# Kernel tuning notes

Measured on AMD Instinct MI355X. Metric: run time of the kernel, lower is better.

The kernel has to match this reference:

```python
import jax, jax.numpy as jnp
import numpy as np
import math

C = 512
D = C // 4  # 128
SCALE = math.sqrt(D)

def setup_inputs() -> dict:
    key = jax.random.key(0)
    k1, k2, k3, k4 = jax.random.split(key, 4)
    x = jax.random.normal(k1, (8, C, 2048), dtype=jnp.float32)
    # q_conv and k_conv share the same weight (tied in the torch module)
    wqk = jax.random.normal(k2, (D, C), dtype=jnp.float32) * (1.0 / math.sqrt(C))
    wv = jax.random.normal(k3, (D, C), dtype=jnp.float32) * (1.0 / math.sqrt(C))
    bv = jax.random.normal(k4, (D,), dtype=jnp.float32) * 0.01
    return {"x": x, "wqk": wqk, "wv": wv, "bv": bv}

def reference(x, wqk, wv, bv):
    # x: [B, C, N]; 1x1 conv == matmul over channel dim
    xq = jnp.einsum('dc,bcn->bnd', wqk, x)          # [B, N, D]
    xk = jnp.einsum('dc,bcn->bdn', wqk, x)          # [B, D, N]
    xv = jnp.einsum('dc,bcn->bdn', wv, x) + bv[None, :, None]  # [B, D, N]
    energy = jnp.einsum('bnd,bdm->bnm', xq, xk) / SCALE  # [B, N, N]
    attention = jax.nn.softmax(energy, axis=-1)
    x_r = jnp.einsum('bdn,bnm->bdm', xv, attention)  # [B, D, N]
    return x_r
```

## Files before the change

kernel.cpp:

```cpp
#include <hip/hip_runtime.h>

typedef short short4v __attribute__((ext_vector_type(4)));
typedef short short8 __attribute__((ext_vector_type(8)));
typedef float floatx4 __attribute__((ext_vector_type(4)));
typedef unsigned int uint;
typedef unsigned short ushort;

#define CH 512
#define NN 2048
#define DD 128
#define RSCALE 0.08838834764831845f

__device__ __forceinline__ float bf2f(ushort u) {
    union { uint i; float f; } v; v.i = ((uint)u) << 16; return v.f;
}
__device__ __forceinline__ ushort f2bf(float f) {
    union { float f; uint u; } v; v.f = f;
    uint u = v.u;
    return (ushort)((u + 0x7fffu + ((u >> 16) & 1u)) >> 16);
}

__global__ __launch_bounds__(256) void k0_prep(
    const float* __restrict__ wqk, const float* __restrict__ wv,
    ushort* __restrict__ Wbf, float* __restrict__ lsum,
    float* __restrict__ out)
{
    int gid = blockIdx.x * 256 + threadIdx.x;
    if (gid < 32768) {
        int base = gid * 4;
        const float* src = (base < 65536) ? (wqk + base) : (wv + base - 65536);
        float4 v = *(const float4*)src;
        short4v o;
        o[0] = (short)f2bf(v.x); o[1] = (short)f2bf(v.y);
        o[2] = (short)f2bf(v.z); o[3] = (short)f2bf(v.w);
        *(short4v*)&Wbf[base] = o;
    }
    if (gid < 16384) lsum[gid] = 0.0f;
    float4 z; z.x = 0.f; z.y = 0.f; z.z = 0.f; z.w = 0.f;
#pragma unroll
    for (int i = 0; i < 4; i++)
        *(float4*)&out[(size_t)(gid + i * 131072) * 4] = z;
}

__global__ __launch_bounds__(256) void k1_proj(
    const float* __restrict__ x,
    const ushort* __restrict__ Wbf,
    const float* __restrict__ bv,
    ushort* __restrict__ Q,
    ushort* __restrict__ VT)
{
    const int nt = blockIdx.x;
    const int h  = blockIdx.y;
    const int b  = blockIdx.z;
    const int n0 = nt * 32;
    const int t = threadIdx.x;
    const int lane = t & 63, w = t >> 6, l15 = lane & 15, quad = lane >> 4;

    __shared__ __attribute__((aligned(16))) ushort As[32 * 72];
    __shared__ __attribute__((aligned(16))) ushort Bs[128 * 72];
    __shared__ __attribute__((aligned(16))) ushort Vt[128 * 40];

    floatx4 acc[2][2];
#pragma unroll
    for (int i = 0; i < 2; i++)
#pragma unroll
        for (int j = 0; j < 2; j++) acc[i][j] = (floatx4)(0.0f);

    const float* xb = x + b * (CH * NN) + n0;
    const ushort* Wh = Wbf + h * 128 * CH;

    const int an = t & 31, ag = t >> 5;

    for (int c0 = 0; c0 < CH; c0 += 64) {
        {
            short8 v;
#pragma unroll
            for (int i = 0; i < 8; i++)
                v[i] = (short)f2bf(xb[(c0 + ag * 8 + i) * NN + an]);
            *(short8*)&As[an * 72 + ag * 8] = v;
        }
#pragma unroll
        for (int rep = 0; rep < 4; rep++) {
            int idx = rep * 256 + t;
            int row = idx >> 3, g = idx & 7;
            *(short8*)&Bs[row * 72 + g * 8] = *(const short8*)&Wh[row * CH + c0 + g * 8];
        }
        __syncthreads();
#pragma unroll
        for (int kd = 0; kd < 2; kd++) {
            short8 a0 = *(short8*)&As[(l15) * 72 + kd * 32 + quad * 8];
            short8 a1 = *(short8*)&As[(16 + l15) * 72 + kd * 32 + quad * 8];
#pragma unroll
            for (int dt2 = 0; dt2 < 2; dt2++) {
                short8 bf = *(short8*)&Bs[(w * 32 + dt2 * 16 + l15) * 72 + kd * 32 + quad * 8];
                acc[0][dt2] = __builtin_amdgcn_mfma_f32_16x16x32_bf16(a0, bf, acc[0][dt2], 0, 0, 0);
                acc[1][dt2] = __builtin_amdgcn_mfma_f32_16x16x32_bf16(a1, bf, acc[1][dt2], 0, 0, 0);
            }
        }
        __syncthreads();
    }

#pragma unroll
    for (int ns = 0; ns < 2; ns++)
#pragma unroll
        for (int dt2 = 0; dt2 < 2; dt2++) {
            int ds_ = w * 32 + dt2 * 16 + l15;
#pragma unroll
            for (int r = 0; r < 4; r++) {
                int nl = ns * 16 + quad * 4 + r;
                float val = acc[ns][dt2][r];
                if (h == 0) {
                    Q[b * (NN * DD) + (n0 + nl) * DD + ds_] = f2bf(val);
                } else {
                    Vt[ds_ * 40 + nl] = f2bf(val + bv[ds_]);
                }
            }
        }
    if (h == 1) {
        __syncthreads();
#pragma unroll
        for (int rep = 0; rep < 2; rep++) {
            int idx = rep * 256 + t;
            int dv = idx >> 2, seg = idx & 3;
            *(short8*)&VT[((size_t)b * DD + dv) * NN + n0 + seg * 8] =
                *(short8*)&Vt[dv * 40 + seg * 8];
        }
    }
}

__global__ __launch_bounds__(256, 4) void k_p(
    const ushort* __restrict__ Q,
    ushort* __restrict__ P,
    float* __restrict__ lsum)
{
    int pid = blockIdx.x;
    const int b = blockIdx.y;
    int it = 0;
    while (pid >= (16 - it)) { pid -= (16 - it); it++; }
    const int jt = it + pid;
    const int i0 = it * 128, j0 = jt * 128;
    const int t = threadIdx.x;
    const int lane = t & 63, w = t >> 6, l15 = lane & 15, quad = lane >> 4;
    const int wi = (w >> 1) * 64, wj = (w & 1) * 64;

    __shared__ __attribute__((aligned(16))) char smem[36864];
    ushort* Qi = (ushort*)smem;
    ushort* Qj = (ushort*)(smem + 18432);
    ushort* Pt = (ushort*)smem;

    const ushort* Qb = Q + b * (NN * DD);

    floatx4 acc[4][4];
#pragma unroll
    for (int i = 0; i < 4; i++)
#pragma unroll
        for (int j = 0; j < 4; j++) acc[i][j] = (floatx4)(0.0f);

    for (int kh = 0; kh < 2; kh++) {
        if (kh) __syncthreads();
#pragma unroll
        for (int rep = 0; rep < 4; rep++) {
            int idx = rep * 256 + t;
            int row = idx >> 3, g = idx & 7;
            *(short8*)&Qi[row * 72 + g * 8] = *(const short8*)&Qb[(i0 + row) * DD + kh * 64 + g * 8];
            *(short8*)&Qj[row * 72 + g * 8] = *(const short8*)&Qb[(j0 + row) * DD + kh * 64 + g * 8];
        }
        __syncthreads();

#pragma unroll
        for (int kd = 0; kd < 2; kd++) {
            short8 afr[4], bfr[4];
#pragma unroll
            for (int nt = 0; nt < 4; nt++)
                afr[nt] = *(short8*)&Qi[(wi + nt * 16 + l15) * 72 + kd * 32 + quad * 8];
#pragma unroll
            for (int mt = 0; mt < 4; mt++)
                bfr[mt] = *(short8*)&Qj[(wj + mt * 16 + l15) * 72 + kd * 32 + quad * 8];
#pragma unroll
            for (int nt = 0; nt < 4; nt++)
#pragma unroll
                for (int mt = 0; mt < 4; mt++)
                    acc[nt][mt] = __builtin_amdgcn_mfma_f32_16x16x32_bf16(afr[nt], bfr[mt], acc[nt][mt], 0, 0, 0);
        }
    }

    __syncthreads();

    float cs[4] = {0.f, 0.f, 0.f, 0.f};
#pragma unroll
    for (int nt = 0; nt < 4; nt++) {
        float rs[4] = {0.f, 0.f, 0.f, 0.f};
#pragma unroll
        for (int mt = 0; mt < 4; mt++)
#pragma unroll
            for (int r = 0; r < 4; r++) {
                float p = __expf(acc[nt][mt][r] * RSCALE);
                rs[r] += p;
                cs[mt] += p;
                Pt[(wi + nt * 16 + quad * 4 + r) * 138 + wj + mt * 16 + l15] = f2bf(p);
            }
#pragma unroll
        for (int r = 0; r < 4; r++) {
            float s = rs[r];
            s += __shfl_xor(s, 1);
            s += __shfl_xor(s, 2);
            s += __shfl_xor(s, 4);
            s += __shfl_xor(s, 8);
            if (l15 == 0)
                atomicAdd(&lsum[b * NN + i0 + wi + nt * 16 + quad * 4 + r], s);
        }
    }
    if (it != jt) {
#pragma unroll
        for (int mt = 0; mt < 4; mt++) {
            float s = cs[mt];
            s += __shfl_xor(s, 16);
            s += __shfl_xor(s, 32);
            if (lane < 16)
                atomicAdd(&lsum[b * NN + j0 + wj + mt * 16 + l15], s);
        }
    }
    __syncthreads();

    ushort* Pb = P + (size_t)b * NN * NN;
#pragma unroll
    for (int rep = 0; rep < 8; rep++) {
        int idx = rep * 256 + t;
        int row = idx >> 4, g = idx & 15;
        *(short8*)&Pb[(size_t)(i0 + row) * NN + j0 + g * 8] =
            *(short8*)&Pt[row * 138 + g * 8];
    }

    if (it != jt) {
        __syncthreads();
#pragma unroll
        for (int nt = 0; nt < 4; nt++)
#pragma unroll
            for (int mt = 0; mt < 4; mt++)
#pragma unroll
                for (int r = 0; r < 4; r++) {
                    float p = __expf(acc[nt][mt][r] * RSCALE);
                    Pt[(wj + mt * 16 + l15) * 138 + wi + nt * 16 + quad * 4 + r] = f2bf(p);
                }
        __syncthreads();
#pragma unroll
        for (int rep = 0; rep < 8; rep++) {
            int idx = rep * 256 + t;
            int row = idx >> 4, g = idx & 15;
            *(short8*)&Pb[(size_t)(j0 + row) * NN + i0 + g * 8] =
                *(short8*)&Pt[row * 138 + g * 8];
        }
    }
}

__global__ __launch_bounds__(256) void k_vscale(
    const ushort* __restrict__ VT, const float* __restrict__ lsum,
    ushort* __restrict__ Vsc)
{
    int gid = blockIdx.x * 256 + threadIdx.x;
    size_t idx = (size_t)gid * 8;
    int b = (int)(idx >> 18);
    int n = (int)(idx & (NN - 1));
    short8 v = *(const short8*)&VT[idx];
    float4 l0 = *(const float4*)&lsum[b * NN + n];
    float4 l1 = *(const float4*)&lsum[b * NN + n + 4];
    short8 o;
    o[0] = (short)f2bf(bf2f((ushort)v[0]) / l0.x);
    o[1] = (short)f2bf(bf2f((ushort)v[1]) / l0.y);
    o[2] = (short)f2bf(bf2f((ushort)v[2]) / l0.z);
    o[3] = (short)f2bf(bf2f((ushort)v[3]) / l0.w);
    o[4] = (short)f2bf(bf2f((ushort)v[4]) / l1.x);
    o[5] = (short)f2bf(bf2f((ushort)v[5]) / l1.y);
    o[6] = (short)f2bf(bf2f((ushort)v[6]) / l1.z);
    o[7] = (short)f2bf(bf2f((ushort)v[7]) / l1.w);
    *(short8*)&Vsc[idx] = o;
}

__global__ __launch_bounds__(256, 4) void k_pv(
    const ushort* __restrict__ Vsc,
    const ushort* __restrict__ P,
    float* __restrict__ out)
{
    const int mt = blockIdx.x;
    const int b  = blockIdx.y;
    const int m0 = mt * 32;
    const int t = threadIdx.x;
    const int lane = t & 63, w = t >> 6, l15 = lane & 15, quad = lane >> 4;

    __shared__ __attribute__((aligned(16))) ushort Vs[128 * 72];
    __shared__ __attribute__((aligned(16))) ushort Pp[32 * 72];

    const ushort* Vb = Vsc + (size_t)b * DD * NN;
    const ushort* Pb = P + (size_t)b * NN * NN;

    floatx4 acc[2][2];
#pragma unroll
    for (int i = 0; i < 2; i++)
#pragma unroll
        for (int j = 0; j < 2; j++) acc[i][j] = (floatx4)(0.0f);

    const int vsd = t >> 3, vsg = t & 7;
    const int psr = t >> 3, psg = t & 7;

    short8 vr[4], pr;

#define LOADR(NC)                                                              \
    do {                                                                       \
        _Pragma("unroll")                                                      \
        for (int rep = 0; rep < 4; rep++)                                      \
            vr[rep] = *(const short8*)&Vb[(size_t)(rep * 32 + vsd) * NN + (NC) + vsg * 8]; \
        pr = *(const short8*)&Pb[(size_t)(m0 + psr) * NN + (NC) + psg * 8];    \
    } while (0)

    LOADR(0);

    for (int n0c = 0; n0c < NN; n0c += 64) {
        __syncthreads();
#pragma unroll
        for (int rep = 0; rep < 4; rep++)
            *(short8*)&Vs[(rep * 32 + vsd) * 72 + vsg * 8] = vr[rep];
        *(short8*)&Pp[psr * 72 + psg * 8] = pr;
        __syncthreads();

        if (n0c + 64 < NN) LOADR(n0c + 64);

#pragma unroll
        for (int kn = 0; kn < 2; kn++) {
            short8 va0 = *(short8*)&Vs[(w * 32 + l15) * 72 + kn * 32 + quad * 8];
            short8 va1 = *(short8*)&Vs[(w * 32 + 16 + l15) * 72 + kn * 32 + quad * 8];
#pragma unroll
            for (int mf = 0; mf < 2; mf++) {
                short8 pb = *(short8*)&Pp[(mf * 16 + l15) * 72 + kn * 32 + quad * 8];
                acc[0][mf] = __builtin_amdgcn_mfma_f32_16x16x32_bf16(va0, pb, acc[0][mf], 0, 0, 0);
                acc[1][mf] = __builtin_amdgcn_mfma_f32_16x16x32_bf16(va1, pb, acc[1][mf], 0, 0, 0);
            }
        }
    }
#undef LOADR

    float* ob = out + (size_t)b * DD * NN;
#pragma unroll
    for (int dsub = 0; dsub < 2; dsub++)
#pragma unroll
        for (int mf = 0; mf < 2; mf++)
#pragma unroll
            for (int r = 0; r < 4; r++) {
                int d = w * 32 + dsub * 16 + quad * 4 + r;
                ob[(size_t)d * NN + m0 + mf * 16 + l15] = acc[dsub][mf][r];
            }
}

__global__ __launch_bounds__(256, 4) void kl_sum(
    const ushort* __restrict__ Q,
    float* __restrict__ lsum)
{
    int pid = blockIdx.x;
    const int b = blockIdx.y;
    int it = 0;
    while (pid >= (16 - it)) { pid -= (16 - it); it++; }
    const int jt = it + pid;
    const int i0 = it * 128, j0 = jt * 128;
    const int t = threadIdx.x;
    const int lane = t & 63, w = t >> 6, l15 = lane & 15, quad = lane >> 4;
    const int wi = (w >> 1) * 64, wj = (w & 1) * 64;

    __shared__ __attribute__((aligned(16))) ushort Qi[128 * 72];
    __shared__ __attribute__((aligned(16))) ushort Qj[128 * 72];

    const ushort* Qb = Q + b * (NN * DD);

    floatx4 acc[4][4];
#pragma unroll
    for (int i = 0; i < 4; i++)
#pragma unroll
        for (int j = 0; j < 4; j++) acc[i][j] = (floatx4)(0.0f);

    for (int kh = 0; kh < 2; kh++) {
        if (kh) __syncthreads();
#pragma unroll
        for (int rep = 0; rep < 4; rep++) {
            int idx = rep * 256 + t;
            int row = idx >> 3, g = idx & 7;
            *(short8*)&Qi[row * 72 + g * 8] = *(const short8*)&Qb[(i0 + row) * DD + kh * 64 + g * 8];
            *(short8*)&Qj[row * 72 + g * 8] = *(const short8*)&Qb[(j0 + row) * DD + kh * 64 + g * 8];
        }
        __syncthreads();

#pragma unroll
        for (int kd = 0; kd < 2; kd++) {
            short8 afr[4], bfr[4];
#pragma unroll
            for (int nt = 0; nt < 4; nt++)
                afr[nt] = *(short8*)&Qi[(wi + nt * 16 + l15) * 72 + kd * 32 + quad * 8];
#pragma unroll
            for (int mt = 0; mt < 4; mt++)
                bfr[mt] = *(short8*)&Qj[(wj + mt * 16 + l15) * 72 + kd * 32 + quad * 8];
#pragma unroll
            for (int nt = 0; nt < 4; nt++)
#pragma unroll
                for (int mt = 0; mt < 4; mt++)
                    acc[nt][mt] = __builtin_amdgcn_mfma_f32_16x16x32_bf16(afr[nt], bfr[mt], acc[nt][mt], 0, 0, 0);
        }
    }

    float cs[4] = {0.f, 0.f, 0.f, 0.f};
#pragma unroll
    for (int nt = 0; nt < 4; nt++) {
        float rs[4] = {0.f, 0.f, 0.f, 0.f};
#pragma unroll
        for (int mt = 0; mt < 4; mt++)
#pragma unroll
            for (int r = 0; r < 4; r++) {
                float p = __expf(acc[nt][mt][r] * RSCALE);
                rs[r] += p;
                cs[mt] += p;
            }
#pragma unroll
        for (int r = 0; r < 4; r++) {
            float s = rs[r];
            s += __shfl_xor(s, 1);
            s += __shfl_xor(s, 2);
            s += __shfl_xor(s, 4);
            s += __shfl_xor(s, 8);
            if (l15 == 0)
                atomicAdd(&lsum[b * NN + i0 + wi + nt * 16 + quad * 4 + r], s);
        }
    }
    if (it != jt) {
#pragma unroll
        for (int mt = 0; mt < 4; mt++) {
            float s = cs[mt];
            s += __shfl_xor(s, 16);
            s += __shfl_xor(s, 32);
            if (lane < 16)
                atomicAdd(&lsum[b * NN + j0 + wj + mt * 16 + l15], s);
        }
    }
}

__global__ __launch_bounds__(256, 4) void k_fused_sep(
    const ushort* __restrict__ Q,
    const ushort* __restrict__ VT,
    const float* __restrict__ lsum,
    float* __restrict__ out)
{
    const int mt = blockIdx.x;
    const int h  = blockIdx.y;
    const int b  = blockIdx.z;
    const int m0 = mt * 32;
    const int t = threadIdx.x;
    const int lane = t & 63, w = t >> 6, l15 = lane & 15, quad = lane >> 4;

    __shared__ __attribute__((aligned(16))) ushort Qn[64 * 136];
    __shared__ __attribute__((aligned(16))) ushort Vs[128 * 72];
    __shared__ __attribute__((aligned(16))) ushort Ps[32 * 68];

    const ushort* Qb = Q + b * (NN * DD);
    const ushort* VTb = VT + (size_t)b * DD * NN;
    const float* lb = lsum + b * NN;

#pragma unroll
    for (int rep = 0; rep < 2; rep++) {
        int idx = rep * 256 + t;
        int row = idx >> 4, g = idx & 15;
        *(short8*)&Qn[row * 136 + g * 8] = *(const short8*)&Qb[(m0 + row) * DD + g * 8];
    }
    __syncthreads();

    short8 qm[2][4];
#pragma unroll
    for (int ms = 0; ms < 2; ms++)
#pragma unroll
        for (int kd = 0; kd < 4; kd++)
            qm[ms][kd] = *(short8*)&Qn[(ms * 16 + l15) * 136 + kd * 32 + quad * 8];

    floatx4 acc[2][2];
#pragma unroll
    for (int i = 0; i < 2; i++)
#pragma unroll
        for (int j = 0; j < 2; j++) acc[i][j] = (floatx4)(0.0f);

    const int qsr = t >> 4, qsg = t & 15;
    const int vsd = t >> 3, vsg = t & 7;

    short8 qr[4], vr[4];

#define LOADR(NC)                                                              \
    do {                                                                       \
        _Pragma("unroll")                                                      \
        for (int rep = 0; rep < 4; rep++)                                      \
            qr[rep] = *(const short8*)&Qb[((NC) + rep * 16 + qsr) * DD + qsg * 8]; \
        _Pragma("unroll")                                                      \
        for (int rep = 0; rep < 4; rep++)                                      \
            vr[rep] = *(const short8*)&VTb[(size_t)(rep * 32 + vsd) * NN + (NC) + vsg * 8]; \
    } while (0)

    const int nbeg = h * (NN / 2), nend = nbeg + (NN / 2);

    LOADR(nbeg);

    for (int n0c = nbeg; n0c < nend; n0c += 64) {
        float lw = lb[n0c + w * 16 + l15];
        __syncthreads();
#pragma unroll
        for (int rep = 0; rep < 4; rep++)
            *(short8*)&Qn[(rep * 16 + qsr) * 136 + qsg * 8] = qr[rep];
#pragma unroll
        for (int rep = 0; rep < 4; rep++)
            *(short8*)&Vs[(rep * 32 + vsd) * 72 + vsg * 8] = vr[rep];
        __syncthreads();

        if (n0c + 64 < nend) LOADR(n0c + 64);

        {
            float linv = 1.0f / lw;
            short8 bq[4];
#pragma unroll
            for (int kd = 0; kd < 4; kd++)
                bq[kd] = *(short8*)&Qn[(w * 16 + l15) * 136 + kd * 32 + quad * 8];
#pragma unroll
            for (int ms = 0; ms < 2; ms++) {
                floatx4 s = (floatx4)(0.0f);
#pragma unroll
                for (int kd = 0; kd < 4; kd++)
                    s = __builtin_amdgcn_mfma_f32_16x16x32_bf16(qm[ms][kd], bq[kd], s, 0, 0, 0);
#pragma unroll
                for (int r = 0; r < 4; r++) {
                    float p = __expf(s[r] * RSCALE) * linv;
                    Ps[(ms * 16 + quad * 4 + r) * 68 + w * 16 + l15] = f2bf(p);
                }
            }
        }
        __syncthreads();

#pragma unroll
        for (int kn = 0; kn < 2; kn++) {
            short8 va0 = *(short8*)&Vs[(w * 32 + l15) * 72 + kn * 32 + quad * 8];
            short8 va1 = *(short8*)&Vs[(w * 32 + 16 + l15) * 72 + kn * 32 + quad * 8];
#pragma unroll
            for (int mf = 0; mf < 2; mf++) {
                short8 pb = *(short8*)&Ps[(mf * 16 + l15) * 68 + kn * 32 + quad * 8];
                acc[0][mf] = __builtin_amdgcn_mfma_f32_16x16x32_bf16(va0, pb, acc[0][mf], 0, 0, 0);
                acc[1][mf] = __builtin_amdgcn_mfma_f32_16x16x32_bf16(va1, pb, acc[1][mf], 0, 0, 0);
            }
        }
    }
#undef LOADR

    float* ob = out + (size_t)b * DD * NN;
#pragma unroll
    for (int dsub = 0; dsub < 2; dsub++)
#pragma unroll
        for (int mf = 0; mf < 2; mf++)
#pragma unroll
            for (int r = 0; r < 4; r++) {
                int d = w * 32 + dsub * 16 + quad * 4 + r;
                atomicAdd(&ob[(size_t)d * NN + m0 + mf * 16 + l15], acc[dsub][mf][r]);
            }
}

__global__ __launch_bounds__(256) void k1_fb(
    const float* __restrict__ x, const float* __restrict__ wqk,
    const float* __restrict__ wv, const float* __restrict__ bv,
    ushort* __restrict__ Q, ushort* __restrict__ V)
{
    const int nt = blockIdx.x;
    const int b  = blockIdx.y;
    const int n0 = nt * 32;
    const int t = threadIdx.x;
    const int lane = t & 63, w = t >> 6, l15 = lane & 15, quad = lane >> 4;

    __shared__ __attribute__((aligned(16))) ushort As[32 * 40];
    __shared__ __attribute__((aligned(16))) ushort Bs[256 * 40];

    floatx4 acc[2][4];
#pragma unroll
    for (int i = 0; i < 2; i++)
#pragma unroll
        for (int j = 0; j < 4; j++) acc[i][j] = (floatx4)(0.0f);

    const float* xb = x + b * (CH * NN) + n0;

    for (int c0 = 0; c0 < CH; c0 += 32) {
        {
            int n = t & 31, g = t >> 5;
            short4v v;
#pragma unroll
            for (int i = 0; i < 4; i++)
                v[i] = (short)f2bf(xb[(c0 + g * 4 + i) * NN + n]);
            *(short4v*)&As[n * 40 + g * 4] = v;
        }
#pragma unroll
        for (int rep = 0; rep < 16; rep++) {
            int idx = rep * 256 + t;
            int row = idx >> 4, cp = idx & 15;
            const float* wf = (row < 128) ? (wqk + row * CH) : (wv + (row - 128) * CH);
            uint pack = (uint)f2bf(wf[c0 + cp * 2]) | ((uint)f2bf(wf[c0 + cp * 2 + 1]) << 16);
            *(uint*)&Bs[row * 40 + cp * 2] = pack;
        }
        __syncthreads();
        short8 a0 = *(short8*)&As[(l15) * 40 + quad * 8];
        short8 a1 = *(short8*)&As[(16 + l15) * 40 + quad * 8];
#pragma unroll
        for (int dt2 = 0; dt2 < 4; dt2++) {
            short8 bf = *(short8*)&Bs[(w * 64 + dt2 * 16 + l15) * 40 + quad * 8];
            acc[0][dt2] = __builtin_amdgcn_mfma_f32_16x16x32_bf16(a0, bf, acc[0][dt2], 0, 0, 0);
            acc[1][dt2] = __builtin_amdgcn_mfma_f32_16x16x32_bf16(a1, bf, acc[1][dt2], 0, 0, 0);
        }
        __syncthreads();
    }
#pragma unroll
    for (int ns = 0; ns < 2; ns++)
#pragma unroll
        for (int dt2 = 0; dt2 < 4; dt2++) {
            int ds_ = w * 64 + dt2 * 16 + l15;
#pragma unroll
            for (int r = 0; r < 4; r++) {
                int n = n0 + ns * 16 + quad * 4 + r;
                float val = acc[ns][dt2][r];
                if (ds_ < 128) {
                    Q[b * (NN * DD) + n * DD + ds_] = f2bf(val);
                } else {
                    int dv = ds_ - 128;
                    V[b * (NN * DD) + n * DD + dv] = f2bf(val + bv[dv]);
                }
            }
        }
}

__global__ __launch_bounds__(256) void k2_norm(
    const ushort* __restrict__ Q, ushort* __restrict__ V)
{
    const int ntile = blockIdx.x;
    const int b = blockIdx.y;
    const int n0 = ntile * 64;
    const int t = threadIdx.x;
    const int lane = t & 63, w = t >> 6, l15 = lane & 15, quad = lane >> 4;

    __shared__ __attribute__((aligned(16))) ushort Qs[64 * 136];
    __shared__ __attribute__((aligned(16))) ushort Qm2[64 * 136];

    const ushort* Qb = Q + b * (NN * DD);

#pragma unroll
    for (int rep = 0; rep < 16; rep++) {
        int idx = rep * 256 + t;
        int row = idx >> 6, dp = idx & 63;
        *(uint*)&Qs[row * 136 + dp * 2] = *(const uint*)&Qb[(n0 + row) * DD + dp * 2];
    }
    __syncthreads();

    short8 afr[4];
#pragma unroll
    for (int kd = 0; kd < 4; kd++)
        afr[kd] = *(short8*)&Qs[(w * 16 + l15) * 136 + kd * 32 + quad * 8];

    float sums[4] = {0.f, 0.f, 0.f, 0.f};

    for (int m0 = 0; m0 < NN; m0 += 64) {
#pragma unroll
        for (int rep = 0; rep < 16; rep++) {
            int idx = rep * 256 + t;
            int row = idx >> 6, dp = idx & 63;
            *(uint*)&Qm2[row * 136 + dp * 2] = *(const uint*)&Qb[(m0 + row) * DD + dp * 2];
        }
        __syncthreads();
#pragma unroll
        for (int ct = 0; ct < 4; ct++) {
            floatx4 s = (floatx4)(0.0f);
#pragma unroll
            for (int kd = 0; kd < 4; kd++) {
                short8 bf = *(short8*)&Qm2[(ct * 16 + l15) * 136 + kd * 32 + quad * 8];
                s = __builtin_amdgcn_mfma_f32_16x16x32_bf16(afr[kd], bf, s, 0, 0, 0);
            }
#pragma unroll
            for (int r = 0; r < 4; r++)
                sums[r] += __expf(s[r] * RSCALE);
        }
        __syncthreads();
    }

#pragma unroll
    for (int r = 0; r < 4; r++) {
        float s = sums[r];
        s += __shfl_xor(s, 1);
        s += __shfl_xor(s, 2);
        s += __shfl_xor(s, 4);
        s += __shfl_xor(s, 8);
        sums[r] = s;
    }

    ushort* Vb = V + b * (NN * DD);
#pragma unroll
    for (int r = 0; r < 4; r++) {
        int n = n0 + w * 16 + quad * 4 + r;
        float inv = 1.0f / sums[r];
        short8 vv = *(short8*)&Vb[n * DD + l15 * 8];
        short8 o;
#pragma unroll
        for (int i = 0; i < 8; i++)
            o[i] = (short)f2bf(bf2f((ushort)vv[i]) * inv);
        *(short8*)&Vb[n * DD + l15 * 8] = o;
    }
}

__global__ __launch_bounds__(256) void k3_attn(
    const ushort* __restrict__ Q, const ushort* __restrict__ Vp,
    float* __restrict__ out)
{
    const int mtile = blockIdx.x;
    const int b = blockIdx.y;
    const int m0 = mtile * 64;
    const int t = threadIdx.x;
    const int lane = t & 63, w = t >> 6, l15 = lane & 15, quad = lane >> 4;

    __shared__ __attribute__((aligned(16))) ushort Qs[64 * 136];
    __shared__ __attribute__((aligned(16))) ushort Qn2[32 * 136];
    __shared__ __attribute__((aligned(16))) ushort Vs2[128 * 40];
    __shared__ __attribute__((aligned(16))) ushort Ps2[64 * 40];

    const ushort* Qb = Q + b * (NN * DD);
    const ushort* Vpb = Vp + b * (NN * DD);

#pragma unroll
    for (int rep = 0; rep < 16; rep++) {
        int idx = rep * 256 + t;
        int row = idx >> 6, dp = idx & 63;
        *(uint*)&Qs[row * 136 + dp * 2] = *(const uint*)&Qb[(m0 + row) * DD + dp * 2];
    }
    __syncthreads();

    short8 afr[4];
#pragma unroll
    for (int kd = 0; kd < 4; kd++)
        afr[kd] = *(short8*)&Qs[(w * 16 + l15) * 136 + kd * 32 + quad * 8];

    floatx4 acc[2][4];
#pragma unroll
    for (int s = 0; s < 2; s++)
#pragma unroll
        for (int mt = 0; mt < 4; mt++) acc[s][mt] = (floatx4)(0.0f);

    for (int n0c = 0; n0c < NN; n0c += 32) {
#pragma unroll
        for (int rep = 0; rep < 8; rep++) {
            int idx = rep * 256 + t;
            int row = idx >> 6, dp = idx & 63;
            *(uint*)&Qn2[row * 136 + dp * 2] = *(const uint*)&Qb[(n0c + row) * DD + dp * 2];
        }
#pragma unroll
        for (int rep = 0; rep < 8; rep++) {
            int idx = rep * 256 + t;
            int np = idx >> 7, d = idx & 127;
            uint v0 = Vpb[(n0c + np * 2) * DD + d];
            uint v1 = Vpb[(n0c + np * 2 + 1) * DD + d];
            *(uint*)&Vs2[d * 40 + np * 2] = v0 | (v1 << 16);
        }
        __syncthreads();

#pragma unroll
        for (int nt2 = 0; nt2 < 2; nt2++) {
            floatx4 s = (floatx4)(0.0f);
#pragma unroll
            for (int kd = 0; kd < 4; kd++) {
                short8 bf = *(short8*)&Qn2[(nt2 * 16 + l15) * 136 + kd * 32 + quad * 8];
                s = __builtin_amdgcn_mfma_f32_16x16x32_bf16(afr[kd], bf, s, 0, 0, 0);
            }
#pragma unroll
            for (int r = 0; r < 4; r++) {
                float p = __expf(s[r] * RSCALE);
                Ps2[(w * 16 + quad * 4 + r) * 40 + nt2 * 16 + l15] = f2bf(p);
            }
        }
        __syncthreads();

        short8 pb[4];
#pragma unroll
        for (int mt = 0; mt < 4; mt++)
            pb[mt] = *(short8*)&Ps2[(mt * 16 + l15) * 40 + quad * 8];
#pragma unroll
        for (int sub = 0; sub < 2; sub++) {
            short8 va = *(short8*)&Vs2[(w * 32 + sub * 16 + l15) * 40 + quad * 8];
#pragma unroll
            for (int mt = 0; mt < 4; mt++)
                acc[sub][mt] = __builtin_amdgcn_mfma_f32_16x16x32_bf16(va, pb[mt], acc[sub][mt], 0, 0, 0);
        }
        __syncthreads();
    }

    float* ob = out + (size_t)b * DD * NN;
#pragma unroll
    for (int sub = 0; sub < 2; sub++)
#pragma unroll
        for (int mt = 0; mt < 4; mt++)
#pragma unroll
            for (int r = 0; r < 4; r++) {
                int d = w * 32 + sub * 16 + quad * 4 + r;
                int m = m0 + mt * 16 + l15;
                ob[(size_t)d * NN + m] = acc[sub][mt][r];
            }
}

extern "C" void kernel_launch(void* const* d_in, const int* in_sizes, int n_in,
                              void* d_out, int out_size, void* d_ws, size_t ws_size,
                              hipStream_t stream) {
    const float* x   = (const float*)d_in[0];
    const float* wqk = (const float*)d_in[1];
    const float* wv  = (const float*)d_in[2];
    const float* bv  = (const float*)d_in[3];
    float* out = (float*)d_out;

    ushort* Q = (ushort*)d_ws;

    if (ws_size >= ((size_t)80 << 20)) {
        ushort* VT   = (ushort*)((char*)d_ws + (4u << 20));
        ushort* Wbf  = (ushort*)((char*)d_ws + (8u << 20));
        float*  lsum = (float*)((char*)d_ws + (8u << 20) + (256u << 10));
        ushort* Vsc  = (ushort*)((char*)d_ws + (9u << 20));
        ushort* P    = (ushort*)((char*)d_ws + (16u << 20));

        k0_prep<<<512, 256, 0, stream>>>(wqk, wv, Wbf, lsum, out);
        k1_proj<<<dim3(64, 2, 8), 256, 0, stream>>>(x, Wbf, bv, Q, VT);
        k_p<<<dim3(136, 8), 256, 0, stream>>>(Q, P, lsum);
        k_vscale<<<1024, 256, 0, stream>>>(VT, lsum, Vsc);
        k_pv<<<dim3(64, 8), 256, 0, stream>>>(Vsc, P, out);
    } else if (ws_size >= (size_t)33 * 1024 * 1024) {
        ushort* VT   = (ushort*)((char*)d_ws + (4u << 20));
        ushort* Wbf  = (ushort*)((char*)d_ws + (8u << 20));
        float*  lsum = (float*)((char*)d_ws + (8u << 20) + (256u << 10));

        k0_prep<<<512, 256, 0, stream>>>(wqk, wv, Wbf, lsum, out);
        k1_proj<<<dim3(64, 2, 8), 256, 0, stream>>>(x, Wbf, bv, Q, VT);
        kl_sum<<<dim3(136, 8), 256, 0, stream>>>(Q, lsum);
        k_fused_sep<<<dim3(64, 2, 8), 256, 0, stream>>>(Q, VT, lsum, out);
    } else {
        ushort* V = (ushort*)((char*)d_ws + (4u << 20));
        k1_fb<<<dim3(64, 8), 256, 0, stream>>>(x, wqk, wv, bv, Q, V);
        k2_norm<<<dim3(32, 8), 256, 0, stream>>>(Q, V);
        k3_attn<<<dim3(32, 8), 256, 0, stream>>>(Q, V, out);
    }
}
```

Before: 149.9 us.

## Fold weight conversion and V normalization into projection and PV kernels

Drops the k0_prep and k_vscale launches on the large-workspace path. Weights are now converted from fp32 to bf16 inside k1_proj, which also zeroes lsum from one block per batch. k_pv loads lsum alongside V tiles and scales V by the reciprocal row sum before writing to shared memory. This removes two launches and the extra VT/Vsc round trip through memory, at the cost of redundant weight conversion per block and extra ALU work in the PV loop. Output zeroing in k0_prep is no longer done on this path, which is fine if k_pv writes out with plain stores.

```diff
diff --git a/kernel.cpp b/kernel.cpp
--- a/kernel.cpp
+++ b/kernel.cpp
@@ -44,10 +44,12 @@
 
 __global__ __launch_bounds__(256) void k1_proj(
     const float* __restrict__ x,
-    const ushort* __restrict__ Wbf,
+    const float* __restrict__ wqk,
+    const float* __restrict__ wv,
     const float* __restrict__ bv,
     ushort* __restrict__ Q,
-    ushort* __restrict__ VT)
+    ushort* __restrict__ VT,
+    float* __restrict__ lsum)
 {
     const int nt = blockIdx.x;
     const int h  = blockIdx.y;
@@ -56,6 +58,12 @@
     const int t = threadIdx.x;
     const int lane = t & 63, w = t >> 6, l15 = lane & 15, quad = lane >> 4;
 
+    if (h == 0 && nt == 0) {
+        float4 z; z.x = 0.f; z.y = 0.f; z.z = 0.f; z.w = 0.f;
+        *(float4*)&lsum[b * NN + t * 8] = z;
+        *(float4*)&lsum[b * NN + t * 8 + 4] = z;
+    }
+
     __shared__ __attribute__((aligned(16))) ushort As[32 * 72];
     __shared__ __attribute__((aligned(16))) ushort Bs[128 * 72];
     __shared__ __attribute__((aligned(16))) ushort Vt[128 * 40];
@@ -67,7 +75,7 @@
         for (int j = 0; j < 2; j++) acc[i][j] = (floatx4)(0.0f);
 
     const float* xb = x + b * (CH * NN) + n0;
-    const ushort* Wh = Wbf + h * 128 * CH;
+    const float* Wh = h ? wv : wqk;
 
     const int an = t & 31, ag = t >> 5;
 
@@ -83,7 +91,15 @@
         for (int rep = 0; rep < 4; rep++) {
             int idx = rep * 256 + t;
             int row = idx >> 3, g = idx & 7;
-            *(short8*)&Bs[row * 72 + g * 8] = *(const short8*)&Wh[row * CH + c0 + g * 8];
+            const float* src = Wh + row * CH + c0 + g * 8;
+            float4 w0 = *(const float4*)src;
+            float4 w1 = *(const float4*)(src + 4);
+            short8 o;
+            o[0] = (short)f2bf(w0.x); o[1] = (short)f2bf(w0.y);
+            o[2] = (short)f2bf(w0.z); o[3] = (short)f2bf(w0.w);
+            o[4] = (short)f2bf(w1.x); o[5] = (short)f2bf(w1.y);
+            o[6] = (short)f2bf(w1.z); o[7] = (short)f2bf(w1.w);
+            *(short8*)&Bs[row * 72 + g * 8] = o;
         }
         __syncthreads();
 #pragma unroll
@@ -253,32 +269,10 @@
     }
 }
 
-__global__ __launch_bounds__(256) void k_vscale(
-    const ushort* __restrict__ VT, const float* __restrict__ lsum,
-    ushort* __restrict__ Vsc)
-{
-    int gid = blockIdx.x * 256 + threadIdx.x;
-    size_t idx = (size_t)gid * 8;
-    int b = (int)(idx >> 18);
-    int n = (int)(idx & (NN - 1));
-    short8 v = *(const short8*)&VT[idx];
-    float4 l0 = *(const float4*)&lsum[b * NN + n];
-    float4 l1 = *(const float4*)&lsum[b * NN + n + 4];
-    short8 o;
-    o[0] = (short)f2bf(bf2f((ushort)v[0]) / l0.x);
-    o[1] = (short)f2bf(bf2f((ushort)v[1]) / l0.y);
-    o[2] = (short)f2bf(bf2f((ushort)v[2]) / l0.z);
-    o[3] = (short)f2bf(bf2f((ushort)v[3]) / l0.w);
-    o[4] = (short)f2bf(bf2f((ushort)v[4]) / l1.x);
-    o[5] = (short)f2bf(bf2f((ushort)v[5]) / l1.y);
-    o[6] = (short)f2bf(bf2f((ushort)v[6]) / l1.z);
-    o[7] = (short)f2bf(bf2f((ushort)v[7]) / l1.w);
-    *(short8*)&Vsc[idx] = o;
-}
-
 __global__ __launch_bounds__(256, 4) void k_pv(
-    const ushort* __restrict__ Vsc,
+    const ushort* __restrict__ VT,
     const ushort* __restrict__ P,
+    const float* __restrict__ lsum,
     float* __restrict__ out)
 {
     const int mt = blockIdx.x;
@@ -290,8 +284,9 @@
     __shared__ __attribute__((aligned(16))) ushort Vs[128 * 72];
     __shared__ __attribute__((aligned(16))) ushort Pp[32 * 72];
 
-    const ushort* Vb = Vsc + (size_t)b * DD * NN;
+    const ushort* Vb = VT + (size_t)b * DD * NN;
     const ushort* Pb = P + (size_t)b * NN * NN;
+    const float* lb = lsum + b * NN;
 
     floatx4 acc[2][2];
 #pragma unroll
@@ -303,6 +298,7 @@
     const int psr = t >> 3, psg = t & 7;
 
     short8 vr[4], pr;
+    float4 lr0, lr1;
 
 #define LOADR(NC)                                                              \
     do {                                                                       \
@@ -310,15 +306,30 @@
         for (int rep = 0; rep < 4; rep++)                                      \
             vr[rep] = *(const short8*)&Vb[(size_t)(rep * 32 + vsd) * NN + (NC) + vsg * 8]; \
         pr = *(const short8*)&Pb[(size_t)(m0 + psr) * NN + (NC) + psg * 8];    \
+        lr0 = *(const float4*)&lb[(NC) + vsg * 8];                             \
+        lr1 = *(const float4*)&lb[(NC) + vsg * 8 + 4];                         \
     } while (0)
 
     LOADR(0);
 
     for (int n0c = 0; n0c < NN; n0c += 64) {
         __syncthreads();
-#pragma unroll
-        for (int rep = 0; rep < 4; rep++)
-            *(short8*)&Vs[(rep * 32 + vsd) * 72 + vsg * 8] = vr[rep];
+        {
+            float li[8];
+            li[0] = 1.0f / lr0.x; li[1] = 1.0f / lr0.y;
+            li[2] = 1.0f / lr0.z; li[3] = 1.0f / lr0.w;
+            li[4] = 1.0f / lr1.x; li[5] = 1.0f / lr1.y;
+            li[6] = 1.0f / lr1.z; li[7] = 1.0f / lr1.w;
+#pragma unroll
+            for (int rep = 0; rep < 4; rep++) {
+                short8 v = vr[rep];
+                short8 o;
+#pragma unroll
+                for (int i = 0; i < 8; i++)
+                    o[i] = (short)f2bf(bf2f((ushort)v[i]) * li[i]);
+                *(short8*)&Vs[(rep * 32 + vsd) * 72 + vsg * 8] = o;
+            }
+        }
         *(short8*)&Pp[psr * 72 + psg * 8] = pr;
         __syncthreads();
 
@@ -814,23 +825,19 @@
 
     if (ws_size >= ((size_t)80 << 20)) {
         ushort* VT   = (ushort*)((char*)d_ws + (4u << 20));
-        ushort* Wbf  = (ushort*)((char*)d_ws + (8u << 20));
         float*  lsum = (float*)((char*)d_ws + (8u << 20) + (256u << 10));
-        ushort* Vsc  = (ushort*)((char*)d_ws + (9u << 20));
         ushort* P    = (ushort*)((char*)d_ws + (16u << 20));
 
-        k0_prep<<<512, 256, 0, stream>>>(wqk, wv, Wbf, lsum, out);
-        k1_proj<<<dim3(64, 2, 8), 256, 0, stream>>>(x, Wbf, bv, Q, VT);
+        k1_proj<<<dim3(64, 2, 8), 256, 0, stream>>>(x, wqk, wv, bv, Q, VT, lsum);
         k_p<<<dim3(136, 8), 256, 0, stream>>>(Q, P, lsum);
-        k_vscale<<<1024, 256, 0, stream>>>(VT, lsum, Vsc);
-        k_pv<<<dim3(64, 8), 256, 0, stream>>>(Vsc, P, out);
+        k_pv<<<dim3(64, 8), 256, 0, stream>>>(VT, P, lsum, out);
     } else if (ws_size >= (size_t)33 * 1024 * 1024) {
         ushort* VT   = (ushort*)((char*)d_ws + (4u << 20));
         ushort* Wbf  = (ushort*)((char*)d_ws + (8u << 20));
         float*  lsum = (float*)((char*)d_ws + (8u << 20) + (256u << 10));
 
         k0_prep<<<512, 256, 0, stream>>>(wqk, wv, Wbf, lsum, out);
-        k1_proj<<<dim3(64, 2, 8), 256, 0, stream>>>(x, Wbf, bv, Q, VT);
+        k1_proj<<<dim3(64, 2, 8), 256, 0, stream>>>(x, wqk, wv, bv, Q, VT, lsum);
         kl_sum<<<dim3(136, 8), 256, 0, stream>>>(Q, lsum);
         k_fused_sep<<<dim3(64, 2, 8), 256, 0, stream>>>(Q, VT, lsum, out);
     } else {
```

Result: slower. 172.1 us (+14.8%).
